# Optimization experiments

Measured on AMD Instinct MI355X. Metric: run time of the kernel, lower is better.

## Reference

```python
import jax, jax.numpy as jnp
import numpy as np

B, S, D, H, DI, L = 16, 80, 512, 64, 2048, 6  # batch, seq, d_model, d_lstm(=d_v), d_inner, n_layers
EPS = 1e-6


def _layer_norm(x, g, b):
    m = jnp.mean(x, axis=-1, keepdims=True)
    v = jnp.mean((x - m) ** 2, axis=-1, keepdims=True)
    return (x - m) * jax.lax.rsqrt(v + EPS) * g + b


def _lstm_last(gx, whh):
    # gx: [T, N, 4H] precomputed input-to-gate projections (bias=False LSTM)
    N = gx.shape[1]
    Hh = whh.shape[1]
    init = (jnp.zeros((N, Hh), gx.dtype), jnp.zeros((N, Hh), gx.dtype))

    def step(carry, g_in):
        h, c = carry
        gates = g_in + h @ whh.T  # [N, 4H], torch gate order i,f,g,o
        i, f, g, o = jnp.split(gates, 4, axis=-1)
        c = jax.nn.sigmoid(f) * c + jax.nn.sigmoid(i) * jnp.tanh(g)
        h = jax.nn.sigmoid(o) * jnp.tanh(c)
        return (h, c), None

    (h, _), _ = jax.lax.scan(step, init, gx)
    return h  # [N, H]


def _perm_indices():
    # deterministic janossy permutation: identity with position i swapped to last
    idx = np.arange(S)
    P = np.tile(idx, (S, 1))
    P[idx, idx] = S - 1
    P[idx, S - 1] = idx
    return jnp.asarray(P)  # [S, S]


def _janossy_layer(q, g, b, wih, whh, wfc, P):
    # q: [B, S, D]
    x = _layer_norm(q, g, b)
    # project inputs to gates once, then gather permutations of the projection
    xg = jnp.einsum('bsd,gd->sbg', x, wih)  # [S, B, 4H]
    pg = xg[P]  # [S_i, S_t, B, 4H]: for each output position i, the permuted sequence
    pg = pg.transpose(1, 0, 2, 3).reshape(S, S * B, 4 * H)  # time-major, fold i into batch
    h = _lstm_last(pg, whh)  # [S*B, H]
    h = h.reshape(S, B, H).transpose(1, 0, 2)  # [B, S, H]
    return h @ wfc.T + q  # fc (dropout=identity in eval) + residual


def _ffn(q, g, b, w1, b1, w2, b2):
    x = _layer_norm(q, g, b)
    return jax.nn.relu(x @ w1.T + b1) @ w2.T + b2 + q


def setup_inputs() -> dict:
    key = jax.random.key(0)
    ks = jax.random.split(key, 10)
    n = lambda k, s, sc: jax.random.normal(k, s, jnp.float32) * sc
    return {
        'src_seq': jax.random.normal(ks[0], (B, S, D), jnp.float32),
        'trg_seq': jax.random.normal(ks[1], (B, S, D), jnp.float32),
        'ln1_g': jnp.ones((L, D), jnp.float32),
        'ln1_b': jnp.zeros((L, D), jnp.float32),
        'wih': n(ks[2], (L, 4 * H, D), 0.04),
        'whh': n(ks[3], (L, 4 * H, H), 0.1),
        'wfc': n(ks[4], (L, D, H), 0.05),
        'ln2_g': jnp.ones((L, D), jnp.float32),
        'ln2_b': jnp.zeros((L, D), jnp.float32),
        'w1': n(ks[5], (L, DI, D), 0.03),
        'b1': jnp.zeros((L, DI), jnp.float32),
        'w2': n(ks[6], (L, D, DI), 0.02),
        'b2': jnp.zeros((L, D), jnp.float32),
        'lnf_g': jnp.ones((D,), jnp.float32),
        'lnf_b': jnp.zeros((D,), jnp.float32),
        'wprj': n(ks[7], (1, D), 0.05),
    }


def reference(src_seq, trg_seq, ln1_g, ln1_b, wih, whh, wfc, ln2_g, ln2_b,
              w1, b1, w2, b2, lnf_g, lnf_b, wprj):
    P = _perm_indices()
    x = src_seq
    for l in range(L):  # small fixed layer count
        x = _janossy_layer(x, ln1_g[l], ln1_b[l], wih[l], whh[l], wfc[l], P)
        x = _ffn(x, ln2_g[l], ln2_b[l], w1[l], b1[l], w2[l], b2[l])
    x = _layer_norm(x, lnf_g, lnf_b)
    seq_logit = x @ wprj.T  # [B, S, 1]
    return seq_logit
```

## Files before the change

### kernel.cpp

```cpp
#include <hip/hip_runtime.h>
#include <hip/hip_bf16.h>

#define B_ 16
#define S_ 80
#define D_ 512
#define H_ 64
#define DI_ 2048
#define L_ 6
#define G4H 256
#define NROW (B_ * S_)
#define EPS_ 1e-6f

typedef __attribute__((ext_vector_type(8))) short short8;
typedef __attribute__((ext_vector_type(4))) float f32x4;

__device__ __forceinline__ float sigmoidf_(float x) {
    return __fdividef(1.0f, 1.0f + __expf(-x));
}
__device__ __forceinline__ float tanh_(float x) {
    return __fdividef(2.0f, 1.0f + __expf(-2.0f * x)) - 1.0f;
}
__device__ __forceinline__ short f2bf(float f) {
    __hip_bfloat16 h = __float2bfloat16(f);
    return *reinterpret_cast<short*>(&h);
}

__global__ __launch_bounds__(256)
void ln_kernel(const float* __restrict__ x, const float* __restrict__ g,
               const float* __restrict__ b, __hip_bfloat16* __restrict__ out) {
    int row = blockIdx.x;
    int t = threadIdx.x;
    const float* xr = x + (size_t)row * D_;
    float v0 = xr[t], v1 = xr[t + 256];
    __shared__ float red[256];
    red[t] = v0 + v1;
    __syncthreads();
    for (int o = 128; o > 0; o >>= 1) { if (t < o) red[t] += red[t + o]; __syncthreads(); }
    float m = red[0] * (1.0f / (float)D_);
    __syncthreads();
    float d0 = v0 - m, d1 = v1 - m;
    red[t] = d0 * d0 + d1 * d1;
    __syncthreads();
    for (int o = 128; o > 0; o >>= 1) { if (t < o) red[t] += red[t + o]; __syncthreads(); }
    float rs = rsqrtf(red[0] * (1.0f / (float)D_) + EPS_);
    __hip_bfloat16* orow = out + (size_t)row * D_;
    orow[t]       = __float2bfloat16(d0 * rs * g[t]       + b[t]);
    orow[t + 256] = __float2bfloat16(d1 * rs * g[t + 256] + b[t + 256]);
}

template<int WITH_BIAS, int WITH_RELU, int WITH_RES, int OUT_MODE>
__global__ __launch_bounds__(256)
void mfma_gemm(const __hip_bfloat16* __restrict__ A, const float* __restrict__ W,
               const float* __restrict__ bias, const float* __restrict__ res,
               void* __restrict__ C, int M, int N, int K) {
    const int LDT = 72;
    __shared__ short As[64 * LDT];
    __shared__ short Ws[64 * LDT];

    int tid  = threadIdx.x;
    int wave = tid >> 6, lane = tid & 63;
    int quad = lane >> 4, l16 = lane & 15;
    int m_off = (wave >> 1) * 32, n_off = (wave & 1) * 32;
    int m0 = blockIdx.y * 64, n0 = blockIdx.x * 64;

    int r = tid >> 2, c = tid & 3;
    const short* Ag = reinterpret_cast<const short*>(A);

    f32x4 acc00 = {0.f,0.f,0.f,0.f}, acc01 = acc00, acc10 = acc00, acc11 = acc00;

    short8 avA[2], avW[2];
    auto load_tile = [&](int k0) {
        const short* arow = &Ag[(size_t)(m0 + r) * K + k0 + c * 16];
        avA[0] = *reinterpret_cast<const short8*>(arow);
        avA[1] = *reinterpret_cast<const short8*>(arow + 8);
        const float* wrow = &W[(size_t)(n0 + r) * K + k0 + c * 16];
        #pragma unroll
        for (int h = 0; h < 2; h++) {
            float4 x0 = *reinterpret_cast<const float4*>(wrow + h * 8);
            float4 x1 = *reinterpret_cast<const float4*>(wrow + h * 8 + 4);
            short8 v;
            v[0] = f2bf(x0.x); v[1] = f2bf(x0.y); v[2] = f2bf(x0.z); v[3] = f2bf(x0.w);
            v[4] = f2bf(x1.x); v[5] = f2bf(x1.y); v[6] = f2bf(x1.z); v[7] = f2bf(x1.w);
            avW[h] = v;
        }
    };

    load_tile(0);
    for (int k0 = 0; k0 < K; k0 += 64) {
        __syncthreads();
        *reinterpret_cast<short8*>(&As[r * LDT + c * 16])     = avA[0];
        *reinterpret_cast<short8*>(&As[r * LDT + c * 16 + 8]) = avA[1];
        *reinterpret_cast<short8*>(&Ws[r * LDT + c * 16])     = avW[0];
        *reinterpret_cast<short8*>(&Ws[r * LDT + c * 16 + 8]) = avW[1];
        __syncthreads();
        if (k0 + 64 < K) load_tile(k0 + 64);

        #pragma unroll
        for (int kc = 0; kc < 2; kc++) {
            short8 a0 = *reinterpret_cast<const short8*>(&As[(m_off + l16) * LDT + kc * 32 + quad * 8]);
            short8 a1 = *reinterpret_cast<const short8*>(&As[(m_off + 16 + l16) * LDT + kc * 32 + quad * 8]);
            short8 b0 = *reinterpret_cast<const short8*>(&Ws[(n_off + l16) * LDT + kc * 32 + quad * 8]);
            short8 b1 = *reinterpret_cast<const short8*>(&Ws[(n_off + 16 + l16) * LDT + kc * 32 + quad * 8]);
            acc00 = __builtin_amdgcn_mfma_f32_16x16x32_bf16(a0, b0, acc00, 0, 0, 0);
            acc01 = __builtin_amdgcn_mfma_f32_16x16x32_bf16(a0, b1, acc01, 0, 0, 0);
            acc10 = __builtin_amdgcn_mfma_f32_16x16x32_bf16(a1, b0, acc10, 0, 0, 0);
            acc11 = __builtin_amdgcn_mfma_f32_16x16x32_bf16(a1, b1, acc11, 0, 0, 0);
        }
    }

    f32x4 accs[2][2] = {{acc00, acc01}, {acc10, acc11}};
    #pragma unroll
    for (int fi = 0; fi < 2; fi++) {
        #pragma unroll
        for (int fj = 0; fj < 2; fj++) {
            int coln = n0 + n_off + fj * 16 + l16;
            float bv = WITH_BIAS ? bias[coln] : 0.0f;
            #pragma unroll
            for (int rr = 0; rr < 4; rr++) {
                int rowm = m0 + m_off + fi * 16 + quad * 4 + rr;
                float v = accs[fi][fj][rr];
                if (WITH_BIAS) v += bv;
                if (WITH_RELU) v = fmaxf(v, 0.0f);
                if (WITH_RES)  v += res[(size_t)rowm * N + coln];
                if (OUT_MODE == 0) {
                    reinterpret_cast<float*>(C)[(size_t)rowm * N + coln] = v;
                } else if (OUT_MODE == 1) {
                    reinterpret_cast<__hip_bfloat16*>(C)[(size_t)rowm * N + coln] = __float2bfloat16(v);
                } else {
                    int b_ = rowm / S_;
                    int s_ = rowm - b_ * S_;
                    int gate = coln >> 6, u = coln & 63;
                    int cp   = ((u >> 4) * 4 + gate) * 16 + (u & 15);
                    int half = b_ >> 3, b7 = b_ & 7;
                    int slot = (b7 >> 1) * 4 + (b7 & 1);
                    reinterpret_cast<__hip_bfloat16*>(C)[
                        (((size_t)(s_ * 2 + half) * 256 + cp) << 4) + slot] = __float2bfloat16(v);
                }
            }
        }
    }
}

__global__ __launch_bounds__(256)
void lstm_v3_kernel(const __hip_bfloat16* __restrict__ xg4,
                    const float* __restrict__ whh,
                    __hip_bfloat16* __restrict__ hlast) {
    const int i    = blockIdx.x;
    const int bh   = blockIdx.y;
    const int tid  = threadIdx.x;
    const int wave = tid >> 6, lane = tid & 63;
    const int quad = lane >> 4, l16 = lane & 15;
    const int unit = wave * 16 + l16;

    short8 bfrag[4][2];
    #pragma unroll
    for (int g = 0; g < 4; g++) {
        const float* wr = &whh[(size_t)(g * 64 + unit) * H_];
        #pragma unroll
        for (int kc = 0; kc < 2; kc++) {
            float4 x0 = *(const float4*)(wr + kc * 32 + quad * 8);
            float4 x1 = *(const float4*)(wr + kc * 32 + quad * 8 + 4);
            short8 v;
            v[0] = f2bf(x0.x); v[1] = f2bf(x0.y); v[2] = f2bf(x0.z); v[3] = f2bf(x0.w);
            v[4] = f2bf(x1.x); v[5] = f2bf(x1.y); v[6] = f2bf(x1.z); v[7] = f2bf(x1.w);
            bfrag[g][kc] = v;
        }
    }

    short8 aI;
    #pragma unroll
    for (int j = 0; j < 8; j++)
        aI[j] = (quad * 8 + j == l16) ? (short)0x3F80 : (short)0;

    __shared__ __attribute__((aligned(16))) short hsh[2][16][72];
    for (int idx = tid; idx < 2 * 16 * 72; idx += 256)
        reinterpret_cast<short*>(hsh)[idx] = 0;

    float cst[2] = {0.f, 0.f};
    float hvv[2] = {0.f, 0.f};

    const short* xgp = reinterpret_cast<const short*>(xg4);
    size_t xbase[4];
    #pragma unroll
    for (int g = 0; g < 4; g++)
        xbase[g] = ((size_t)bh * 256 + (wave * 4 + g) * 16 + l16) * 16 + (quad & 1) * 8;

    short8 b2[4];
    {
        int s0 = (0 == i) ? (S_ - 1) : 0;
        #pragma unroll
        for (int g = 0; g < 4; g++)
            b2[g] = *reinterpret_cast<const short8*>(&xgp[(size_t)s0 * 8192 + xbase[g]]);
    }

    __syncthreads();

    for (int t = 0; t < S_; t++) {
        const int pb = t & 1;
        short8 af0 = *reinterpret_cast<const short8*>(&hsh[pb][l16][quad * 8]);
        short8 af1 = *reinterpret_cast<const short8*>(&hsh[pb][l16][32 + quad * 8]);

        const f32x4 z4 = {0.f, 0.f, 0.f, 0.f};
        f32x4 acc[4];
        #pragma unroll
        for (int g = 0; g < 4; g++)
            acc[g] = __builtin_amdgcn_mfma_f32_16x16x32_bf16(aI, b2[g], z4, 0, 0, 0);

        if (t + 1 < S_) {
            int tn = t + 1;
            int sn = (tn == i) ? (S_ - 1) : ((tn == S_ - 1) ? i : tn);
            #pragma unroll
            for (int g = 0; g < 4; g++)
                b2[g] = *reinterpret_cast<const short8*>(&xgp[(size_t)sn * 8192 + xbase[g]]);
        }

        #pragma unroll
        for (int g = 0; g < 4; g++) {
            acc[g] = __builtin_amdgcn_mfma_f32_16x16x32_bf16(af0, bfrag[g][0], acc[g], 0, 0, 0);
            acc[g] = __builtin_amdgcn_mfma_f32_16x16x32_bf16(af1, bfrag[g][1], acc[g], 0, 0, 0);
        }

        #pragma unroll
        for (int r = 0; r < 2; r++) {
            float ig = sigmoidf_(acc[0][r]);
            float fg = sigmoidf_(acc[1][r]);
            float gg = tanh_(acc[2][r]);
            float og = sigmoidf_(acc[3][r]);
            float cc = fg * cst[r] + ig * gg;
            cst[r] = cc;
            float h = og * tanh_(cc);
            hvv[r] = h;
            hsh[pb ^ 1][quad * 4 + r][unit] = f2bf(h);
        }
        __syncthreads();
    }

    #pragma unroll
    for (int r = 0; r < 2; r++) {
        int b = bh * 8 + quad * 2 + r;
        hlast[((size_t)b * S_ + i) * H_ + unit] = __float2bfloat16(hvv[r]);
    }
}

__global__ __launch_bounds__(256)
void final_kernel(const float* __restrict__ x, const float* __restrict__ g,
                  const float* __restrict__ b, const float* __restrict__ wprj,
                  float* __restrict__ out) {
    int row = blockIdx.x;
    int t = threadIdx.x;
    const float* xr = x + (size_t)row * D_;
    float v0 = xr[t], v1 = xr[t + 256];
    __shared__ float red[256];
    red[t] = v0 + v1;
    __syncthreads();
    for (int o = 128; o > 0; o >>= 1) { if (t < o) red[t] += red[t + o]; __syncthreads(); }
    float m = red[0] * (1.0f / (float)D_);
    __syncthreads();
    float d0 = v0 - m, d1 = v1 - m;
    red[t] = d0 * d0 + d1 * d1;
    __syncthreads();
    for (int o = 128; o > 0; o >>= 1) { if (t < o) red[t] += red[t + o]; __syncthreads(); }
    float rs = rsqrtf(red[0] * (1.0f / (float)D_) + EPS_);
    __syncthreads();
    float y0 = (d0 * rs * g[t] + b[t]) * wprj[t];
    float y1 = (d1 * rs * g[t + 256] + b[t + 256]) * wprj[t + 256];
    red[t] = y0 + y1;
    __syncthreads();
    for (int o = 128; o > 0; o >>= 1) { if (t < o) red[t] += red[t + o]; __syncthreads(); }
    if (t == 0) out[row] = red[0];
}

extern "C" void kernel_launch(void* const* d_in, const int* in_sizes, int n_in,
                              void* d_out, int out_size, void* d_ws, size_t ws_size,
                              hipStream_t stream) {
    const float* src   = (const float*)d_in[0];
    const float* ln1_g = (const float*)d_in[2];
    const float* ln1_b = (const float*)d_in[3];
    const float* wih   = (const float*)d_in[4];
    const float* whh   = (const float*)d_in[5];
    const float* wfc   = (const float*)d_in[6];
    const float* ln2_g = (const float*)d_in[7];
    const float* ln2_b = (const float*)d_in[8];
    const float* w1    = (const float*)d_in[9];
    const float* b1    = (const float*)d_in[10];
    const float* w2    = (const float*)d_in[11];
    const float* b2    = (const float*)d_in[12];
    const float* lnf_g = (const float*)d_in[13];
    const float* lnf_b = (const float*)d_in[14];
    const float* wprj  = (const float*)d_in[15];
    float* out = (float*)d_out;

    char* ws = (char*)d_ws;
    float* xcur = (float*)ws;                       ws += (size_t)NROW * D_  * 4;
    __hip_bfloat16* lnb = (__hip_bfloat16*)ws;      ws += (size_t)NROW * D_  * 2;
    __hip_bfloat16* xg4 = (__hip_bfloat16*)ws;      ws += (size_t)S_ * 2 * 256 * 16 * 2;
    __hip_bfloat16* hb  = (__hip_bfloat16*)ws;      ws += (size_t)NROW * H_  * 2;
    __hip_bfloat16* f1  = (__hip_bfloat16*)ws;      ws += (size_t)NROW * DI_ * 2;

    hipMemcpyAsync(xcur, src, (size_t)NROW * D_ * sizeof(float),
                   hipMemcpyDeviceToDevice, stream);

    for (int l = 0; l < L_; l++) {
        ln_kernel<<<NROW, 256, 0, stream>>>(xcur, ln1_g + (size_t)l * D_,
                                            ln1_b + (size_t)l * D_, lnb);
        mfma_gemm<0, 0, 0, 2><<<dim3(G4H / 64, NROW / 64), 256, 0, stream>>>(
            lnb, wih + (size_t)l * G4H * D_, nullptr, nullptr, xg4, NROW, G4H, D_);
        lstm_v3_kernel<<<dim3(S_, 2), 256, 0, stream>>>(
            xg4, whh + (size_t)l * G4H * H_, hb);
        mfma_gemm<0, 0, 1, 0><<<dim3(D_ / 64, NROW / 64), 256, 0, stream>>>(
            hb, wfc + (size_t)l * D_ * H_, nullptr, xcur, xcur, NROW, D_, H_);
        ln_kernel<<<NROW, 256, 0, stream>>>(xcur, ln2_g + (size_t)l * D_,
                                            ln2_b + (size_t)l * D_, lnb);
        mfma_gemm<1, 1, 0, 1><<<dim3(DI_ / 64, NROW / 64), 256, 0, stream>>>(
            lnb, w1 + (size_t)l * DI_ * D_, b1 + (size_t)l * DI_, nullptr, f1, NROW, DI_, D_);
        mfma_gemm<1, 0, 1, 0><<<dim3(D_ / 64, NROW / 64), 256, 0, stream>>>(
            f1, w2 + (size_t)l * D_ * DI_, b2 + (size_t)l * D_, xcur, xcur, NROW, D_, DI_);
    }
    final_kernel<<<NROW, 256, 0, stream>>>(xcur, lnf_g, lnf_b, wprj, out);
}
```

Before: 778.7 us.

## Pre-convert weights to bf16, use shuffle LayerNorm, load fp32 LSTM gates directly

Adds a kernel that converts all GEMM weights to bf16 once per call, so GEMM tile loads read bf16 directly instead of converting fp32 in every tile. LayerNorm reductions switch from shared-memory trees to wave shuffles with fewer barriers. The input-gate projection is now written as fp32 in a simpler layout that the LSTM loads straight into its accumulators, replacing the identity-matrix MFMA used to inject it. This trades extra conversion launches and a larger fp32 gate buffer for less per-step and per-tile work.

```diff
diff --git a/kernel.cpp b/kernel.cpp
--- a/kernel.cpp
+++ b/kernel.cpp
@@ -26,23 +26,37 @@
 }
 
 __global__ __launch_bounds__(256)
+void w2bf_kernel(const float* __restrict__ s, __hip_bfloat16* __restrict__ d, int n4) {
+    int i = blockIdx.x * 256 + threadIdx.x;
+    if (i < n4) {
+        float4 v = reinterpret_cast<const float4*>(s)[i];
+        short4 o;
+        o.x = f2bf(v.x); o.y = f2bf(v.y); o.z = f2bf(v.z); o.w = f2bf(v.w);
+        reinterpret_cast<short4*>(d)[i] = o;
+    }
+}
+
+__global__ __launch_bounds__(256)
 void ln_kernel(const float* __restrict__ x, const float* __restrict__ g,
                const float* __restrict__ b, __hip_bfloat16* __restrict__ out) {
     int row = blockIdx.x;
     int t = threadIdx.x;
     const float* xr = x + (size_t)row * D_;
     float v0 = xr[t], v1 = xr[t + 256];
-    __shared__ float red[256];
-    red[t] = v0 + v1;
-    __syncthreads();
-    for (int o = 128; o > 0; o >>= 1) { if (t < o) red[t] += red[t + o]; __syncthreads(); }
-    float m = red[0] * (1.0f / (float)D_);
-    __syncthreads();
+    __shared__ float ws4[4], qs4[4];
+    float s = v0 + v1;
+    #pragma unroll
+    for (int o = 32; o > 0; o >>= 1) s += __shfl_down(s, o);
+    if ((t & 63) == 0) ws4[t >> 6] = s;
+    __syncthreads();
+    float m = (ws4[0] + ws4[1] + ws4[2] + ws4[3]) * (1.0f / (float)D_);
     float d0 = v0 - m, d1 = v1 - m;
-    red[t] = d0 * d0 + d1 * d1;
-    __syncthreads();
-    for (int o = 128; o > 0; o >>= 1) { if (t < o) red[t] += red[t + o]; __syncthreads(); }
-    float rs = rsqrtf(red[0] * (1.0f / (float)D_) + EPS_);
+    float q = d0 * d0 + d1 * d1;
+    #pragma unroll
+    for (int o = 32; o > 0; o >>= 1) q += __shfl_down(q, o);
+    if ((t & 63) == 0) qs4[t >> 6] = q;
+    __syncthreads();
+    float rs = rsqrtf((qs4[0] + qs4[1] + qs4[2] + qs4[3]) * (1.0f / (float)D_) + EPS_);
     __hip_bfloat16* orow = out + (size_t)row * D_;
     orow[t]       = __float2bfloat16(d0 * rs * g[t]       + b[t]);
     orow[t + 256] = __float2bfloat16(d1 * rs * g[t + 256] + b[t + 256]);
@@ -50,7 +64,7 @@
 
 template<int WITH_BIAS, int WITH_RELU, int WITH_RES, int OUT_MODE>
 __global__ __launch_bounds__(256)
-void mfma_gemm(const __hip_bfloat16* __restrict__ A, const float* __restrict__ W,
+void mfma_gemm(const __hip_bfloat16* __restrict__ A, const __hip_bfloat16* __restrict__ W,
                const float* __restrict__ bias, const float* __restrict__ res,
                void* __restrict__ C, int M, int N, int K) {
     const int LDT = 72;
@@ -65,6 +79,7 @@
 
     int r = tid >> 2, c = tid & 3;
     const short* Ag = reinterpret_cast<const short*>(A);
+    const short* Wg = reinterpret_cast<const short*>(W);
 
     f32x4 acc00 = {0.f,0.f,0.f,0.f}, acc01 = acc00, acc10 = acc00, acc11 = acc00;
 
@@ -73,16 +88,9 @@
         const short* arow = &Ag[(size_t)(m0 + r) * K + k0 + c * 16];
         avA[0] = *reinterpret_cast<const short8*>(arow);
         avA[1] = *reinterpret_cast<const short8*>(arow + 8);
-        const float* wrow = &W[(size_t)(n0 + r) * K + k0 + c * 16];
-        #pragma unroll
-        for (int h = 0; h < 2; h++) {
-            float4 x0 = *reinterpret_cast<const float4*>(wrow + h * 8);
-            float4 x1 = *reinterpret_cast<const float4*>(wrow + h * 8 + 4);
-            short8 v;
-            v[0] = f2bf(x0.x); v[1] = f2bf(x0.y); v[2] = f2bf(x0.z); v[3] = f2bf(x0.w);
-            v[4] = f2bf(x1.x); v[5] = f2bf(x1.y); v[6] = f2bf(x1.z); v[7] = f2bf(x1.w);
-            avW[h] = v;
-        }
+        const short* wrow = &Wg[(size_t)(n0 + r) * K + k0 + c * 16];
+        avW[0] = *reinterpret_cast<const short8*>(wrow);
+        avW[1] = *reinterpret_cast<const short8*>(wrow + 8);
     };
 
     load_tile(0);
@@ -130,11 +138,9 @@
                     int b_ = rowm / S_;
                     int s_ = rowm - b_ * S_;
                     int gate = coln >> 6, u = coln & 63;
-                    int cp   = ((u >> 4) * 4 + gate) * 16 + (u & 15);
-                    int half = b_ >> 3, b7 = b_ & 7;
-                    int slot = (b7 >> 1) * 4 + (b7 & 1);
-                    reinterpret_cast<__hip_bfloat16*>(C)[
-                        (((size_t)(s_ * 2 + half) * 256 + cp) << 4) + slot] = __float2bfloat16(v);
+                    int half = b_ >> 3, slot = b_ & 7;
+                    reinterpret_cast<float*>(C)[
+                        ((((size_t)(s_ * 2 + half) * 4 + gate) * 64 + u) << 3) + slot] = v;
                 }
             }
         }
@@ -142,7 +148,7 @@
 }
 
 __global__ __launch_bounds__(256)
-void lstm_v3_kernel(const __hip_bfloat16* __restrict__ xg4,
+void lstm_v4_kernel(const float* __restrict__ xg5,
                     const float* __restrict__ whh,
                     __hip_bfloat16* __restrict__ hlast) {
     const int i    = blockIdx.x;
@@ -167,11 +173,6 @@
         }
     }
 
-    short8 aI;
-    #pragma unroll
-    for (int j = 0; j < 8; j++)
-        aI[j] = (quad * 8 + j == l16) ? (short)0x3F80 : (short)0;
-
     __shared__ __attribute__((aligned(16))) short hsh[2][16][72];
     for (int idx = tid; idx < 2 * 16 * 72; idx += 256)
         reinterpret_cast<short*>(hsh)[idx] = 0;
@@ -179,18 +180,17 @@
     float cst[2] = {0.f, 0.f};
     float hvv[2] = {0.f, 0.f};
 
-    const short* xgp = reinterpret_cast<const short*>(xg4);
-    size_t xbase[4];
+    size_t xoff[4];
     #pragma unroll
     for (int g = 0; g < 4; g++)
-        xbase[g] = ((size_t)bh * 256 + (wave * 4 + g) * 16 + l16) * 16 + (quad & 1) * 8;
-
-    short8 b2[4];
+        xoff[g] = ((((size_t)bh * 4 + g) * 64 + unit) << 3) + quad * 2;
+
+    float2 xv[4];
     {
         int s0 = (0 == i) ? (S_ - 1) : 0;
         #pragma unroll
         for (int g = 0; g < 4; g++)
-            b2[g] = *reinterpret_cast<const short8*>(&xgp[(size_t)s0 * 8192 + xbase[g]]);
+            xv[g] = *reinterpret_cast<const float2*>(&xg5[(size_t)s0 * 4096 + xoff[g]]);
     }
 
     __syncthreads();
@@ -200,18 +200,19 @@
         short8 af0 = *reinterpret_cast<const short8*>(&hsh[pb][l16][quad * 8]);
         short8 af1 = *reinterpret_cast<const short8*>(&hsh[pb][l16][32 + quad * 8]);
 
-        const f32x4 z4 = {0.f, 0.f, 0.f, 0.f};
         f32x4 acc[4];
         #pragma unroll
-        for (int g = 0; g < 4; g++)
-            acc[g] = __builtin_amdgcn_mfma_f32_16x16x32_bf16(aI, b2[g], z4, 0, 0, 0);
+        for (int g = 0; g < 4; g++) {
+            f32x4 a = {xv[g].x, xv[g].y, xv[g].x, xv[g].y};
+            acc[g] = a;
+        }
 
         if (t + 1 < S_) {
             int tn = t + 1;
             int sn = (tn == i) ? (S_ - 1) : ((tn == S_ - 1) ? i : tn);
             #pragma unroll
             for (int g = 0; g < 4; g++)
-                b2[g] = *reinterpret_cast<const short8*>(&xgp[(size_t)sn * 8192 + xbase[g]]);
+                xv[g] = *reinterpret_cast<const float2*>(&xg5[(size_t)sn * 4096 + xoff[g]]);
         }
 
         #pragma unroll
@@ -293,9 +294,25 @@
     char* ws = (char*)d_ws;
     float* xcur = (float*)ws;                       ws += (size_t)NROW * D_  * 4;
     __hip_bfloat16* lnb = (__hip_bfloat16*)ws;      ws += (size_t)NROW * D_  * 2;
-    __hip_bfloat16* xg4 = (__hip_bfloat16*)ws;      ws += (size_t)S_ * 2 * 256 * 16 * 2;
+    float* xg5  = (float*)ws;                       ws += (size_t)S_ * 4096  * 4;
     __hip_bfloat16* hb  = (__hip_bfloat16*)ws;      ws += (size_t)NROW * H_  * 2;
     __hip_bfloat16* f1  = (__hip_bfloat16*)ws;      ws += (size_t)NROW * DI_ * 2;
+    __hip_bfloat16* wihb = (__hip_bfloat16*)ws;     ws += (size_t)L_ * G4H * D_ * 2;
+    __hip_bfloat16* wfcb = (__hip_bfloat16*)ws;     ws += (size_t)L_ * D_ * H_ * 2;
+    __hip_bfloat16* w1b  = (__hip_bfloat16*)ws;     ws += (size_t)L_ * DI_ * D_ * 2;
+    __hip_bfloat16* w2b  = (__hip_bfloat16*)ws;     ws += (size_t)L_ * D_ * DI_ * 2;
+
+    {
+        int n4;
+        n4 = L_ * G4H * D_ / 4;
+        w2bf_kernel<<<(n4 + 255) / 256, 256, 0, stream>>>(wih, wihb, n4);
+        n4 = L_ * D_ * H_ / 4;
+        w2bf_kernel<<<(n4 + 255) / 256, 256, 0, stream>>>(wfc, wfcb, n4);
+        n4 = L_ * DI_ * D_ / 4;
+        w2bf_kernel<<<(n4 + 255) / 256, 256, 0, stream>>>(w1, w1b, n4);
+        n4 = L_ * D_ * DI_ / 4;
+        w2bf_kernel<<<(n4 + 255) / 256, 256, 0, stream>>>(w2, w2b, n4);
+    }
 
     hipMemcpyAsync(xcur, src, (size_t)NROW * D_ * sizeof(float),
                    hipMemcpyDeviceToDevice, stream);
@@ -304,17 +321,17 @@
         ln_kernel<<<NROW, 256, 0, stream>>>(xcur, ln1_g + (size_t)l * D_,
                                             ln1_b + (size_t)l * D_, lnb);
         mfma_gemm<0, 0, 0, 2><<<dim3(G4H / 64, NROW / 64), 256, 0, stream>>>(
-            lnb, wih + (size_t)l * G4H * D_, nullptr, nullptr, xg4, NROW, G4H, D_);
-        lstm_v3_kernel<<<dim3(S_, 2), 256, 0, stream>>>(
-            xg4, whh + (size_t)l * G4H * H_, hb);
+            lnb, wihb + (size_t)l * G4H * D_, nullptr, nullptr, xg5, NROW, G4H, D_);
+        lstm_v4_kernel<<<dim3(S_, 2), 256, 0, stream>>>(
+            xg5, whh + (size_t)l * G4H * H_, hb);
         mfma_gemm<0, 0, 1, 0><<<dim3(D_ / 64, NROW / 64), 256, 0, stream>>>(
-            hb, wfc + (size_t)l * D_ * H_, nullptr, xcur, xcur, NROW, D_, H_);
+            hb, wfcb + (size_t)l * D_ * H_, nullptr, xcur, xcur, NROW, D_, H_);
         ln_kernel<<<NROW, 256, 0, stream>>>(xcur, ln2_g + (size_t)l * D_,
                                             ln2_b + (size_t)l * D_, lnb);
         mfma_gemm<1, 1, 0, 1><<<dim3(DI_ / 64, NROW / 64), 256, 0, stream>>>(
-            lnb, w1 + (size_t)l * DI_ * D_, b1 + (size_t)l * DI_, nullptr, f1, NROW, DI_, D_);
+            lnb, w1b + (size_t)l * DI_ * D_, b1 + (size_t)l * DI_, nullptr, f1, NROW, DI_, D_);
         mfma_gemm<1, 0, 1, 0><<<dim3(D_ / 64, NROW / 64), 256, 0, stream>>>(
-            f1, w2 + (size_t)l * D_ * DI_, b2 + (size_t)l * D_, xcur, xcur, NROW, D_, DI_);
+            f1, w2b + (size_t)l * D_ * DI_, b2 + (size_t)l * D_, xcur, xcur, NROW, D_, DI_);
     }
     final_kernel<<<NROW, 256, 0, stream>>>(xcur, lnf_g, lnf_b, wprj, out);
 }
```

New measurement: 716.4 us. 8.0% less time.
